# Performance work log

Measured on AMD Instinct MI355X. Metric: run time of the kernel, lower is better.

Reference implementation:

```python
import jax, jax.numpy as jnp
import numpy as np

N, D, H = 4096, 1024, 16
HD = D // H  # 64
EPS = 1e-5


def setup_inputs() -> dict:
    key = jax.random.key(0)
    ks = jax.random.split(key, 12)
    lim = 1.0 / np.sqrt(D)
    def lin(kw, kb):
        W = jax.random.uniform(kw, (D, D), jnp.float32, -lim, lim)
        b = jax.random.uniform(kb, (D,), jnp.float32, -lim, lim)
        return W, b
    Wq, bq = lin(ks[0], ks[1])
    Wk, bk = lin(ks[2], ks[3])
    Wv, bv = lin(ks[4], ks[5])
    Wo, bo = lin(ks[6], ks[7])
    return {
        "query": jax.random.normal(ks[8], (N, D), jnp.float32),
        "key": jax.random.normal(ks[9], (N, D), jnp.float32),
        "value": jax.random.normal(ks[10], (N, D), jnp.float32),
        "Wq": Wq, "bq": bq, "Wk": Wk, "bk": bk,
        "Wv": Wv, "bv": bv, "Wo": Wo, "bo": bo,
        "q_norm_w": jnp.ones((HD,), jnp.float32),
        "k_norm_w": jnp.ones((HD,), jnp.float32),
    }


def _rmsnorm(x, w):
    # eqx.nn.RMSNorm: weight-only, eps=1e-5, over last dim
    inv = jax.lax.rsqrt(jnp.mean(x * x, axis=-1, keepdims=True) + EPS)
    return w * x * inv


def reference(query, key, value, Wq, bq, Wk, bk, Wv, bv, Wo, bo, q_norm_w, k_norm_w):
    n = query.shape[0]
    q = (query @ Wq.T + bq).reshape(n, H, HD)
    k = (key @ Wk.T + bk).reshape(n, H, HD)
    v = (value @ Wv.T + bv).reshape(n, H, HD)
    q = _rmsnorm(q, q_norm_w)
    k = _rmsnorm(k, k_norm_w)
    # scale=1.0: raw unscaled dot-product logits
    logits = jnp.einsum('qhd,khd->hqk', q, k)  # [H, N, N]
    probs = jax.nn.softmax(logits, axis=-1)
    attn = jnp.einsum('hqk,khd->qhd', probs, v).reshape(n, H * HD)
    return attn @ Wo.T + bo
```

## Files before the change

### kernel.cpp

```cpp
#include <hip/hip_runtime.h>
#include <stdint.h>
#include <stddef.h>

#define N_TOK 4096
#define DM    1024
#define NHEAD 16
#define HD    64

typedef __attribute__((ext_vector_type(8)))  short bf16x8;
typedef __attribute__((ext_vector_type(4)))  short bf16x4;
typedef __attribute__((ext_vector_type(4)))  float f32x4;
typedef __attribute__((ext_vector_type(16))) float f32x16;

static __device__ __forceinline__ float bf2f(short u) {
  union { unsigned int i; float f; } c;
  c.i = ((unsigned int)(unsigned short)u) << 16;
  return c.f;
}
static __device__ __forceinline__ unsigned short f2bf(float f) {
  union { float f; unsigned int i; } c; c.f = f;
  unsigned int x = c.i;
  return (unsigned short)((x + 0x7fffu + ((x >> 16) & 1u)) >> 16);
}
static __device__ __forceinline__ unsigned int cvtpk(float lo, float hi) {
  unsigned int d;
  asm("v_cvt_pk_bf16_f32 %0, %1, %2" : "=v"(d) : "v"(lo), "v"(hi));
  return d;
}
static __device__ __forceinline__ void plswap(unsigned int& a, unsigned int& b) {
  asm("v_permlane32_swap_b32 %0, %1" : "+v"(a), "+v"(b));
}
#if __has_builtin(__builtin_amdgcn_exp2f)
#define EXP2(x) __builtin_amdgcn_exp2f(x)
#else
#define EXP2(x) exp2f(x)
#endif
static __device__ __forceinline__ void gload16(const void* g, void* l) {
  __builtin_amdgcn_global_load_lds(
      (const __attribute__((address_space(1))) unsigned int*)g,
      (__attribute__((address_space(3))) unsigned int*)l, 16, 0, 0);
}

struct Cvt7 { const float* s[7]; unsigned short* d[7]; };
__global__ void cvt_all(Cvt7 a) {
  int u0 = blockIdx.x << 10;
  int seg, off;
  if (u0 < 1572864) { seg = u0 >> 19; off = u0 & 524287; }
  else { int j = u0 - 1572864; seg = 3 + (j >> 17); off = j & 131071; }
  const float* s = a.s[seg];
  unsigned short* dd = a.d[seg];
  int t = off + threadIdx.x;
#pragma unroll
  for (int j = 0; j < 4; ++j, t += 256) {
    const f32x4* sp = (const f32x4*)(s + (size_t)t * 8);
    f32x4 x = sp[0], y = sp[1];
    bf16x8 o;
    o[0] = (short)f2bf(x[0]); o[1] = (short)f2bf(x[1]);
    o[2] = (short)f2bf(x[2]); o[3] = (short)f2bf(x[3]);
    o[4] = (short)f2bf(y[0]); o[5] = (short)f2bf(y[1]);
    o[6] = (short)f2bf(y[2]); o[7] = (short)f2bf(y[3]);
    *(bf16x8*)(dd + (size_t)t * 8) = o;
  }
}

template <int MI>
static __device__ __forceinline__ void gemm_core(
    const unsigned short* __restrict__ A,
    const unsigned short* __restrict__ W,
    const float* __restrict__ bias,
    unsigned short* __restrict__ Cb,
    float* __restrict__ Cf,
    const float* __restrict__ nw,
    int Nn, int K, int mode, int m0, int n0)
{
  __shared__ __align__(16) unsigned short At[2][MI * 1024];
  __shared__ __align__(16) unsigned short Wt[2][128 * 32];
  const int tid  = threadIdx.x;
  const int wid  = tid >> 6, lane = tid & 63;
  const int lm   = lane & 15, lg = lane >> 4;
  const int wm   = (wid >> 1) * (MI * 16), wn = (wid & 1) * 64;
  const int CPW  = (MI * 2 + 8) / 4;

  f32x4 acc[MI][4];
#pragma unroll
  for (int i = 0; i < MI; ++i)
#pragma unroll
    for (int j = 0; j < 4; ++j) acc[i][j] = f32x4{0.f, 0.f, 0.f, 0.f};

  auto stage = [&](int b, int k0) {
#pragma unroll
    for (int i = 0; i < CPW; ++i) {
      int c = wid * CPW + i;
      if (c < MI * 2)
        gload16(A + (size_t)(m0 + c * 16 + (lane >> 2)) * K + k0 + (lane & 3) * 8,
                (char*)At + b * (MI * 2048) + c * 1024);
      else
        gload16(W + (size_t)(n0 + (c - MI * 2) * 16 + (lane >> 2)) * K + k0 + (lane & 3) * 8,
                (char*)Wt + b * 8192 + (c - MI * 2) * 1024);
    }
  };

  const int nk = K >> 5;
  stage(0, 0);
  __syncthreads();
  for (int kt = 0; kt < nk; ++kt) {
    const int cur = kt & 1;
    if (kt + 1 < nk) stage(cur ^ 1, (kt + 1) << 5);

    bf16x8 af[MI], bfr[4];
#pragma unroll
    for (int mi = 0; mi < MI; ++mi)
      af[mi] = *(const bf16x8*)&At[cur][(wm + mi * 16 + lm) * 32 + lg * 8];
#pragma unroll
    for (int ni = 0; ni < 4; ++ni)
      bfr[ni] = *(const bf16x8*)&Wt[cur][(wn + ni * 16 + lm) * 32 + lg * 8];
    __builtin_amdgcn_s_setprio(1);
#pragma unroll
    for (int mi = 0; mi < MI; ++mi)
#pragma unroll
      for (int ni = 0; ni < 4; ++ni)
        acc[mi][ni] = __builtin_amdgcn_mfma_f32_16x16x32_bf16(
            af[mi], bfr[ni], acc[mi][ni], 0, 0, 0);
    __builtin_amdgcn_s_setprio(0);
    __syncthreads();
  }

  float bv[4];
#pragma unroll
  for (int ni = 0; ni < 4; ++ni) bv[ni] = bias[n0 + wn + ni * 16 + lm];

  if (mode <= 1) {
#pragma unroll
    for (int mi = 0; mi < MI; ++mi)
#pragma unroll
      for (int ni = 0; ni < 4; ++ni) {
        int n = n0 + wn + ni * 16 + lm;
#pragma unroll
        for (int r = 0; r < 4; ++r) {
          int m = m0 + wm + mi * 16 + lg * 4 + r;
          float v = acc[mi][ni][r] + bv[ni];
          if (mode == 1) Cf[(size_t)m * Nn + n] = v;
          else           Cb[(size_t)m * Nn + n] = f2bf(v);
        }
      }
  } else if (mode == 2) {
    const int h = (n0 + wn) >> 6;
    float w_[4];
#pragma unroll
    for (int ni = 0; ni < 4; ++ni) w_[ni] = nw[ni * 16 + lm];
#pragma unroll
    for (int mi = 0; mi < MI; ++mi) {
      float t[4][4], ssq[4];
#pragma unroll
      for (int ni = 0; ni < 4; ++ni)
#pragma unroll
        for (int r = 0; r < 4; ++r) t[ni][r] = acc[mi][ni][r] + bv[ni];
#pragma unroll
      for (int r = 0; r < 4; ++r)
        ssq[r] = t[0][r]*t[0][r] + t[1][r]*t[1][r] + t[2][r]*t[2][r] + t[3][r]*t[3][r];
#pragma unroll
      for (int r = 0; r < 4; ++r) {
        ssq[r] += __shfl_xor(ssq[r], 1);
        ssq[r] += __shfl_xor(ssq[r], 2);
        ssq[r] += __shfl_xor(ssq[r], 4);
        ssq[r] += __shfl_xor(ssq[r], 8);
      }
#pragma unroll
      for (int r = 0; r < 4; ++r) {
        float iv = rsqrtf(ssq[r] * (1.f / 64.f) + 1e-5f);
        int n_ = m0 + wm + mi * 16 + lg * 4 + r;
#pragma unroll
        for (int ni = 0; ni < 4; ++ni) {
          int d = ni * 16 + lm;
          Cb[(size_t)h * (N_TOK * HD) + (size_t)n_ * HD + d] = f2bf(t[ni][r] * w_[ni] * iv);
        }
      }
    }
  } else {
    const int h = (n0 + wn) >> 6;
#pragma unroll
    for (int mi = 0; mi < MI; ++mi)
#pragma unroll
      for (int ni = 0; ni < 4; ++ni) {
        int d  = ni * 16 + lm;
        int nb = m0 + wm + mi * 16 + lg * 4;
        bf16x4 o;
#pragma unroll
        for (int r = 0; r < 4; ++r) o[r] = (short)f2bf(acc[mi][ni][r] + bv[ni]);
        *(bf16x4*)&Cb[(size_t)h * (HD * N_TOK) + (size_t)d * N_TOK + nb] = o;
      }
  }
}

__global__ __launch_bounds__(256, 3) void qkv_gemm(
    const unsigned short* __restrict__ a0, const unsigned short* __restrict__ a1,
    const unsigned short* __restrict__ a2,
    const unsigned short* __restrict__ w0, const unsigned short* __restrict__ w1,
    const unsigned short* __restrict__ w2,
    const float* __restrict__ b0, const float* __restrict__ b1,
    const float* __restrict__ b2,
    unsigned short* __restrict__ o0, unsigned short* __restrict__ o1,
    unsigned short* __restrict__ o2,
    const float* __restrict__ knw)
{
  const int z = blockIdx.z;
  const unsigned short* A = (z == 0) ? a0 : (z == 1) ? a1 : a2;
  const unsigned short* W = (z == 0) ? w0 : (z == 1) ? w1 : w2;
  const float* B          = (z == 0) ? b0 : (z == 1) ? b1 : b2;
  unsigned short* O       = (z == 0) ? o0 : (z == 1) ? o1 : o2;
  const int mode          = (z == 0) ? 0 : (z == 1) ? 2 : 3;
  gemm_core<4>(A, W, B, O, nullptr, knw, DM, DM, mode,
               blockIdx.y * 128, blockIdx.x * 128);
}

__global__ __launch_bounds__(256, 3) void out_gemm(
    const unsigned short* __restrict__ A, const unsigned short* __restrict__ W,
    const float* __restrict__ bias, float* __restrict__ Cf)
{
  gemm_core<4>(A, W, bias, nullptr, Cf, nullptr, DM, DM, 1,
               blockIdx.y * 128, blockIdx.x * 128);
}

__global__ __launch_bounds__(512, 4) void attn_kernel(
    const unsigned short* __restrict__ qb,
    const unsigned short* __restrict__ kn,
    const unsigned short* __restrict__ vt,
    const float* __restrict__ wq,
    unsigned short* __restrict__ ob)
{
  __shared__ __align__(16) unsigned short SM[2][2][2][4096];

  const int wg   = blockIdx.x;
  const int x_   = wg & 7, rest = wg >> 3;
  const int h    = x_ * 2 + (rest & 1);
  const int qt   = rest >> 1;
  const int tid  = threadIdx.x;
  const int wid  = tid >> 6, lane = tid & 63;
  const int g    = wid >> 2, wv = wid & 3;
  const int l31  = lane & 31, hi = lane >> 5;
  const int sl   = l31 & 7;
  const int qbase = qt * 128 + wv * 32;

  bf16x8 qf[4];
  {
    const unsigned short* qp = qb + (size_t)(qbase + l31) * DM + h * HD + hi * 8;
    float qv[32]; float ss = 0.f;
#pragma unroll
    for (int s = 0; s < 4; ++s) {
      bf16x8 raw = *(const bf16x8*)(qp + s * 16);
#pragma unroll
      for (int j = 0; j < 8; ++j) { float f = bf2f(raw[j]); qv[s*8+j] = f; ss += f*f; }
    }
    ss += __shfl_xor(ss, 32);
    float inv = rsqrtf(ss * (1.f / 64.f) + 1e-5f) * 1.44269504f;
#pragma unroll
    for (int s = 0; s < 4; ++s)
#pragma unroll
      for (int j = 0; j < 8; ++j)
        qf[s][j] = (short)f2bf(qv[s*8+j] * wq[s*16 + hi*8 + j] * inv);
  }

  int slot[4];
#pragma unroll
  for (int x = 0; x < 4; ++x) slot[x] = (((2*x + hi) ^ sl) << 4);
  const char* base = (const char*)SM + g * 32768 + l31 * 128;

  const char* gsrc[4];
  char*       ldst[4];
  long        gstep[4];
  {
    const char* knb = (const char*)kn + (size_t)h * (N_TOK * HD * 2);
    const char* vtb = (const char*)vt + (size_t)h * (HD * N_TOK * 2);
    char* smG = (char*)SM + g * 32768;
#pragma unroll
    for (int i = 0; i < 4; ++i) {
      int chunk = wv * 4 + i;
      int off   = (chunk & 7) * 1024 + lane * 16;
      int row   = off >> 7;
      int scol  = (off & 127) ^ ((row & 7) << 4);
      if (chunk < 8) {
        gsrc[i]  = knb + (size_t)(g * 2048 + row) * 128 + scol;
        gstep[i] = 64 * 128;
        ldst[i]  = smG + (chunk & 7) * 1024;
      } else {
        gsrc[i]  = vtb + (size_t)row * (N_TOK * 2) + g * 4096 + scol;
        gstep[i] = 64 * 2;
        ldst[i]  = smG + 8192 + (chunk & 7) * 1024;
      }
    }
  }

  f32x16 oacc[2], fz;
#pragma unroll
  for (int r = 0; r < 16; ++r) { oacc[0][r] = 0.f; oacc[1][r] = 0.f; fz[r] = 0.f; }
  float lsp[4] = {0.f, 0.f, 0.f, 0.f};

#pragma unroll
  for (int i = 0; i < 4; ++i) { gload16(gsrc[i], ldst[i]); gsrc[i] += gstep[i]; }
  __syncthreads();

  const int NT = 2048 / 64;
  for (int it = 0; it < NT; ++it) {
    const int cur = it & 1;
    if (it + 1 < NT) {
      const int nb = cur ^ 1;
#pragma unroll
      for (int i = 0; i < 4; ++i) {
        gload16(gsrc[i], ldst[i] + nb * 16384);
        gsrc[i] += gstep[i];
      }
    }
    const char* KB = base + cur * 16384;
    const char* VB = KB + 8192;

#pragma unroll
    for (int kt = 0; kt < 2; ++kt) {
      __builtin_amdgcn_s_setprio(1);
      bf16x8 kf0 = *(const bf16x8*)(KB + kt * 4096 + slot[0]);
      f32x16 sc = __builtin_amdgcn_mfma_f32_32x32x16_bf16(kf0, qf[0], fz, 0, 0, 0);
#pragma unroll
      for (int s = 1; s < 4; ++s) {
        bf16x8 kf = *(const bf16x8*)(KB + kt * 4096 + slot[s]);
        sc = __builtin_amdgcn_mfma_f32_32x32x16_bf16(kf, qf[s], sc, 0, 0, 0);
      }
      __builtin_amdgcn_s_setprio(0);
      float e[16];
#pragma unroll
      for (int r = 0; r < 16; ++r) { e[r] = EXP2(sc[r]); lsp[r & 3] += e[r]; }
      unsigned int wpk[4][2];
#pragma unroll
      for (int b = 0; b < 4; ++b) {
        wpk[b][0] = cvtpk(e[4*b+0], e[4*b+1]);
        wpk[b][1] = cvtpk(e[4*b+2], e[4*b+3]);
      }
#pragma unroll
      for (int pr = 0; pr < 2; ++pr) {
        unsigned int x0 = wpk[2*pr][0], x1 = wpk[2*pr][1];
        unsigned int y0 = wpk[2*pr+1][0], y1 = wpk[2*pr+1][1];
        plswap(x0, y0);
        plswap(x1, y1);
        union { unsigned int u[4]; bf16x8 v; } pa;
        pa.u[0] = x0; pa.u[1] = x1; pa.u[2] = y0; pa.u[3] = y1;
        int ks = kt * 2 + pr;
        __builtin_amdgcn_s_setprio(1);
#pragma unroll
        for (int dt = 0; dt < 2; ++dt) {
          bf16x8 vf = *(const bf16x8*)(VB + dt * 4096 + slot[ks]);
          oacc[dt] = __builtin_amdgcn_mfma_f32_32x32x16_bf16(pa.v, vf, oacc[dt], 0, 0, 0);
        }
        __builtin_amdgcn_s_setprio(0);
      }
    }
    __syncthreads();
  }

  float ls = (lsp[0] + lsp[1]) + (lsp[2] + lsp[3]);
  ls += __shfl_xor(ls, 32);

  float* ex  = (float*)((char*)SM + 32768);
  float* lsx = (float*)SM;
  const int idx = wv * 64 + lane;
  if (g == 1) {
#pragma unroll
    for (int dt = 0; dt < 2; ++dt)
#pragma unroll
      for (int r = 0; r < 16; ++r)
        ex[(dt * 16 + r) * 256 + idx] = oacc[dt][r];
    lsx[idx] = ls;
  }
  __syncthreads();
  if (g == 0) {
#pragma unroll
    for (int dt = 0; dt < 2; ++dt)
#pragma unroll
      for (int r = 0; r < 16; ++r)
        oacc[dt][r] += ex[(dt * 16 + r) * 256 + idx];
    ls += lsx[idx];
    float il = 1.f / ls;
#pragma unroll
    for (int r = 0; r < 16; ++r) {
      int q = (r & 3) + 8 * (r >> 2) + 4 * hi;
      float ilr = __int_as_float(
          __builtin_amdgcn_ds_bpermute(q << 2, __float_as_int(il)));
      unsigned short* op = ob + (size_t)(qbase + q) * DM + h * HD + l31;
      op[0]  = f2bf(oacc[0][r] * ilr);
      op[32] = f2bf(oacc[1][r] * ilr);
    }
  }
}

extern "C" void kernel_launch(void* const* d_in, const int* in_sizes, int n_in,
                              void* d_out, int out_size, void* d_ws, size_t ws_size,
                              hipStream_t stream) {
  const float* query = (const float*)d_in[0];
  const float* key   = (const float*)d_in[1];
  const float* value = (const float*)d_in[2];
  const float* Wq    = (const float*)d_in[3];
  const float* bq    = (const float*)d_in[4];
  const float* Wk    = (const float*)d_in[5];
  const float* bk    = (const float*)d_in[6];
  const float* Wv    = (const float*)d_in[7];
  const float* bv    = (const float*)d_in[8];
  const float* Wo    = (const float*)d_in[9];
  const float* bo    = (const float*)d_in[10];
  const float* qnw   = (const float*)d_in[11];
  const float* knw   = (const float*)d_in[12];

  char* ws = (char*)d_ws;
  const size_t MB = 1024 * 1024;
  unsigned short* qpj = (unsigned short*)(ws + 0 * MB);
  unsigned short* Kn  = (unsigned short*)(ws + 8 * MB);
  unsigned short* Vt  = (unsigned short*)(ws + 16 * MB);
  unsigned short* wob = (unsigned short*)(ws + 24 * MB);
  unsigned short* wqb = (unsigned short*)(ws + 26 * MB);
  unsigned short* wkb = (unsigned short*)(ws + 28 * MB);
  unsigned short* wvb = (unsigned short*)(ws + 30 * MB);
  unsigned short* qbf = (unsigned short*)(ws + 32 * MB);
  unsigned short* kbf = (unsigned short*)(ws + 40 * MB);
  unsigned short* vbf = (unsigned short*)(ws + 48 * MB);
  unsigned short* apj = (unsigned short*)(ws + 56 * MB);

  Cvt7 ca;
  ca.s[0] = query; ca.d[0] = qbf;
  ca.s[1] = key;   ca.d[1] = kbf;
  ca.s[2] = value; ca.d[2] = vbf;
  ca.s[3] = Wq;    ca.d[3] = wqb;
  ca.s[4] = Wk;    ca.d[4] = wkb;
  ca.s[5] = Wv;    ca.d[5] = wvb;
  ca.s[6] = Wo;    ca.d[6] = wob;
  cvt_all<<<2048, 256, 0, stream>>>(ca);

  qkv_gemm<<<dim3(DM / 128, N_TOK / 128, 3), 256, 0, stream>>>(
      qbf, kbf, vbf, wqb, wkb, wvb, bq, bk, bv, qpj, Kn, Vt, knw);

  attn_kernel<<<512, 512, 0, stream>>>(qpj, Kn, Vt, qnw, apj);

  out_gemm<<<dim3(DM / 128, N_TOK / 128), 256, 0, stream>>>(apj, wob, bo, (float*)d_out);
}
```

Measured before the change: 152.2 us.

## Split attention KV range across separate blocks and merge partials in new kernel

Attention workgroups no longer hold two 4-wave groups that split the KV range and reduce through shared memory. Each 256-thread block now handles one KV half, so twice as many smaller blocks launch, and unnormalized bf16 partial outputs and row sums go to workspace. A new merge kernel adds the two partials and normalizes them. The aim is higher occupancy and no in-block reduction barrier, at the cost of an extra launch, extra global traffic for the partials, and rounding the partials to bf16 before the sum.

```diff
diff --git a/kernel.cpp b/kernel.cpp
--- a/kernel.cpp
+++ b/kernel.cpp
@@ -221,25 +221,26 @@
                blockIdx.y * 128, blockIdx.x * 128);
 }
 
-__global__ __launch_bounds__(512, 4) void attn_kernel(
+__global__ __launch_bounds__(256, 5) void attn_kernel(
     const unsigned short* __restrict__ qb,
     const unsigned short* __restrict__ kn,
     const unsigned short* __restrict__ vt,
     const float* __restrict__ wq,
-    unsigned short* __restrict__ ob)
+    unsigned short* __restrict__ opart,
+    float* __restrict__ lpart)
 {
-  __shared__ __align__(16) unsigned short SM[2][2][2][4096];
+  __shared__ __align__(16) unsigned short SM[2][2][4096];
 
   const int wg   = blockIdx.x;
   const int x_   = wg & 7, rest = wg >> 3;
   const int h    = x_ * 2 + (rest & 1);
-  const int qt   = rest >> 1;
+  const int sp   = (rest >> 1) & 1;
+  const int qt   = rest >> 2;
   const int tid  = threadIdx.x;
   const int wid  = tid >> 6, lane = tid & 63;
-  const int g    = wid >> 2, wv = wid & 3;
   const int l31  = lane & 31, hi = lane >> 5;
   const int sl   = l31 & 7;
-  const int qbase = qt * 128 + wv * 32;
+  const int qbase = qt * 128 + wid * 32;
 
   bf16x8 qf[4];
   {
@@ -263,7 +264,7 @@
   int slot[4];
 #pragma unroll
   for (int x = 0; x < 4; ++x) slot[x] = (((2*x + hi) ^ sl) << 4);
-  const char* base = (const char*)SM + g * 32768 + l31 * 128;
+  const char* base = (const char*)SM + l31 * 128;
 
   const char* gsrc[4];
   char*       ldst[4];
@@ -271,21 +272,20 @@
   {
     const char* knb = (const char*)kn + (size_t)h * (N_TOK * HD * 2);
     const char* vtb = (const char*)vt + (size_t)h * (HD * N_TOK * 2);
-    char* smG = (char*)SM + g * 32768;
 #pragma unroll
     for (int i = 0; i < 4; ++i) {
-      int chunk = wv * 4 + i;
+      int chunk = wid * 4 + i;
       int off   = (chunk & 7) * 1024 + lane * 16;
       int row   = off >> 7;
       int scol  = (off & 127) ^ ((row & 7) << 4);
       if (chunk < 8) {
-        gsrc[i]  = knb + (size_t)(g * 2048 + row) * 128 + scol;
+        gsrc[i]  = knb + (size_t)(sp * 2048 + row) * 128 + scol;
         gstep[i] = 64 * 128;
-        ldst[i]  = smG + (chunk & 7) * 1024;
+        ldst[i]  = (char*)SM + (chunk & 7) * 1024;
       } else {
-        gsrc[i]  = vtb + (size_t)row * (N_TOK * 2) + g * 4096 + scol;
+        gsrc[i]  = vtb + (size_t)row * (N_TOK * 2) + sp * 4096 + scol;
         gstep[i] = 64 * 2;
-        ldst[i]  = smG + 8192 + (chunk & 7) * 1024;
+        ldst[i]  = (char*)SM + 8192 + (chunk & 7) * 1024;
       }
     }
   }
@@ -356,37 +356,33 @@
 
   float ls = (lsp[0] + lsp[1]) + (lsp[2] + lsp[3]);
   ls += __shfl_xor(ls, 32);
-
-  float* ex  = (float*)((char*)SM + 32768);
-  float* lsx = (float*)SM;
-  const int idx = wv * 64 + lane;
-  if (g == 1) {
-#pragma unroll
-    for (int dt = 0; dt < 2; ++dt)
-#pragma unroll
-      for (int r = 0; r < 16; ++r)
-        ex[(dt * 16 + r) * 256 + idx] = oacc[dt][r];
-    lsx[idx] = ls;
-  }
-  __syncthreads();
-  if (g == 0) {
-#pragma unroll
-    for (int dt = 0; dt < 2; ++dt)
-#pragma unroll
-      for (int r = 0; r < 16; ++r)
-        oacc[dt][r] += ex[(dt * 16 + r) * 256 + idx];
-    ls += lsx[idx];
-    float il = 1.f / ls;
-#pragma unroll
-    for (int r = 0; r < 16; ++r) {
-      int q = (r & 3) + 8 * (r >> 2) + 4 * hi;
-      float ilr = __int_as_float(
-          __builtin_amdgcn_ds_bpermute(q << 2, __float_as_int(il)));
-      unsigned short* op = ob + (size_t)(qbase + q) * DM + h * HD + l31;
-      op[0]  = f2bf(oacc[0][r] * ilr);
-      op[32] = f2bf(oacc[1][r] * ilr);
-    }
-  }
+  unsigned short* Opb = opart + (size_t)sp * (N_TOK * DM);
+#pragma unroll
+  for (int r = 0; r < 16; ++r) {
+    int q = (r & 3) + 8 * (r >> 2) + 4 * hi;
+    unsigned short* p = Opb + (size_t)(qbase + q) * DM + h * HD + l31;
+    p[0]  = f2bf(oacc[0][r]);
+    p[32] = f2bf(oacc[1][r]);
+  }
+  if (hi == 0)
+    lpart[(size_t)sp * (NHEAD * N_TOK) + h * N_TOK + qbase + l31] = ls;
+}
+
+__global__ void merge_kernel(const unsigned short* __restrict__ opart,
+                             const float* __restrict__ lpart,
+                             unsigned short* __restrict__ am)
+{
+  int i = (blockIdx.x * 256 + threadIdx.x) * 8;
+  int n = i >> 10, c = i & 1023, h = c >> 6;
+  float l = lpart[h * N_TOK + n] + lpart[NHEAD * N_TOK + h * N_TOK + n];
+  float il = 1.f / l;
+  bf16x8 a = *(const bf16x8*)(opart + (size_t)n * DM + c);
+  bf16x8 b = *(const bf16x8*)(opart + (size_t)(N_TOK * DM) + (size_t)n * DM + c);
+  bf16x8 o;
+#pragma unroll
+  for (int j = 0; j < 8; ++j)
+    o[j] = (short)f2bf((bf2f(a[j]) + bf2f(b[j])) * il);
+  *(bf16x8*)(am + i) = o;
 }
 
 extern "C" void kernel_launch(void* const* d_in, const int* in_sizes, int n_in,
@@ -419,6 +415,8 @@
   unsigned short* kbf = (unsigned short*)(ws + 40 * MB);
   unsigned short* vbf = (unsigned short*)(ws + 48 * MB);
   unsigned short* apj = (unsigned short*)(ws + 56 * MB);
+  unsigned short* Op  = (unsigned short*)(ws + 32 * MB);
+  float*          Lp  = (float*)(ws + 48 * MB);
 
   Cvt7 ca;
   ca.s[0] = query; ca.d[0] = qbf;
@@ -433,7 +431,9 @@
   qkv_gemm<<<dim3(DM / 128, N_TOK / 128, 3), 256, 0, stream>>>(
       qbf, kbf, vbf, wqb, wkb, wvb, bq, bk, bv, qpj, Kn, Vt, knw);
 
-  attn_kernel<<<512, 512, 0, stream>>>(qpj, Kn, Vt, qnw, apj);
+  attn_kernel<<<1024, 256, 0, stream>>>(qpj, Kn, Vt, qnw, Op, Lp);
+
+  merge_kernel<<<N_TOK * DM / 8 / 256, 256, 0, stream>>>(Op, Lp, apj);
 
   out_gemm<<<dim3(DM / 128, N_TOK / 128), 256, 0, stream>>>(apj, wob, bo, (float*)d_out);
 }
```

After: 168.3 us. 10.6% more time.

## Fuse fp32-to-bf16 activation conversion into QKV GEMM tile loads

Applied to the files above, without the earlier changes.

The QKV projection GEMM now loads fp32 query/key/value tiles straight into LDS using an XOR-swizzled layout and converts them to bf16 in registers with v_cvt_pk_bf16_f32 before the MFMA. The standalone conversion kernel now only handles the four weight matrices. This drops one full read and write pass over the 48 MB of activations. In exchange the A tile in LDS is twice as large, which may lower occupancy, and the GEMM loads twice the A bytes from global memory, since each tile is re-read for every N block.

```diff
diff --git a/kernel.cpp b/kernel.cpp
--- a/kernel.cpp
+++ b/kernel.cpp
@@ -41,12 +41,10 @@
       (__attribute__((address_space(3))) unsigned int*)l, 16, 0, 0);
 }
 
-struct Cvt7 { const float* s[7]; unsigned short* d[7]; };
-__global__ void cvt_all(Cvt7 a) {
+struct Cvt4 { const float* s[4]; unsigned short* d[4]; };
+__global__ void cvt_w(Cvt4 a) {
   int u0 = blockIdx.x << 10;
-  int seg, off;
-  if (u0 < 1572864) { seg = u0 >> 19; off = u0 & 524287; }
-  else { int j = u0 - 1572864; seg = 3 + (j >> 17); off = j & 131071; }
+  int seg = u0 >> 17, off = u0 & 131071;
   const float* s = a.s[seg];
   unsigned short* dd = a.d[seg];
   int t = off + threadIdx.x;
@@ -63,9 +61,10 @@
   }
 }
 
-template <int MI>
+template <int MI, bool AF32>
 static __device__ __forceinline__ void gemm_core(
     const unsigned short* __restrict__ A,
+    const float* __restrict__ A32,
     const unsigned short* __restrict__ W,
     const float* __restrict__ bias,
     unsigned short* __restrict__ Cb,
@@ -73,13 +72,15 @@
     const float* __restrict__ nw,
     int Nn, int K, int mode, int m0, int n0)
 {
-  __shared__ __align__(16) unsigned short At[2][MI * 1024];
+  __shared__ __align__(16) unsigned short At[2][MI * (AF32 ? 2048 : 1024)];
   __shared__ __align__(16) unsigned short Wt[2][128 * 32];
   const int tid  = threadIdx.x;
   const int wid  = tid >> 6, lane = tid & 63;
   const int lm   = lane & 15, lg = lane >> 4;
   const int wm   = (wid >> 1) * (MI * 16), wn = (wid & 1) * 64;
-  const int CPW  = (MI * 2 + 8) / 4;
+  const int NCA  = AF32 ? MI * 4 : MI * 2;
+  const int CPW  = (NCA + 8) / 4;
+  const int ABUF = MI * (AF32 ? 4096 : 2048);
 
   f32x4 acc[MI][4];
 #pragma unroll
@@ -91,12 +92,22 @@
 #pragma unroll
     for (int i = 0; i < CPW; ++i) {
       int c = wid * CPW + i;
-      if (c < MI * 2)
-        gload16(A + (size_t)(m0 + c * 16 + (lane >> 2)) * K + k0 + (lane & 3) * 8,
-                (char*)At + b * (MI * 2048) + c * 1024);
-      else
-        gload16(W + (size_t)(n0 + (c - MI * 2) * 16 + (lane >> 2)) * K + k0 + (lane & 3) * 8,
-                (char*)Wt + b * 8192 + (c - MI * 2) * 1024);
+      if (c < NCA) {
+        if constexpr (AF32) {
+          int off  = c * 1024 + lane * 16;
+          int row  = off >> 7;
+          int scol = (off & 127) ^ ((row & 7) << 4);
+          gload16(A32 + (size_t)(m0 + row) * K + k0 + (scol >> 2),
+                  (char*)At + b * ABUF + c * 1024);
+        } else {
+          gload16(A + (size_t)(m0 + c * 16 + (lane >> 2)) * K + k0 + (lane & 3) * 8,
+                  (char*)At + b * ABUF + c * 1024);
+        }
+      } else {
+        int cw = c - NCA;
+        gload16(W + (size_t)(n0 + cw * 16 + (lane >> 2)) * K + k0 + (lane & 3) * 8,
+                (char*)Wt + b * 8192 + cw * 1024);
+      }
     }
   };
 
@@ -109,8 +120,21 @@
 
     bf16x8 af[MI], bfr[4];
 #pragma unroll
-    for (int mi = 0; mi < MI; ++mi)
-      af[mi] = *(const bf16x8*)&At[cur][(wm + mi * 16 + lm) * 32 + lg * 8];
+    for (int mi = 0; mi < MI; ++mi) {
+      if constexpr (AF32) {
+        int arow = wm + mi * 16 + lm;
+        const char* ab = (char*)At + cur * ABUF + arow * 128;
+        int swz = (arow & 7) << 4;
+        f32x4 a0 = *(const f32x4*)(ab + ((lg * 32) ^ swz));
+        f32x4 a1 = *(const f32x4*)(ab + ((lg * 32 + 16) ^ swz));
+        union { unsigned int u[4]; bf16x8 v; } p;
+        p.u[0] = cvtpk(a0[0], a0[1]); p.u[1] = cvtpk(a0[2], a0[3]);
+        p.u[2] = cvtpk(a1[0], a1[1]); p.u[3] = cvtpk(a1[2], a1[3]);
+        af[mi] = p.v;
+      } else {
+        af[mi] = *(const bf16x8*)&At[cur][(wm + mi * 16 + lm) * 32 + lg * 8];
+      }
+    }
 #pragma unroll
     for (int ni = 0; ni < 4; ++ni)
       bfr[ni] = *(const bf16x8*)&Wt[cur][(wn + ni * 16 + lm) * 32 + lg * 8];
@@ -193,8 +217,8 @@
 }
 
 __global__ __launch_bounds__(256, 3) void qkv_gemm(
-    const unsigned short* __restrict__ a0, const unsigned short* __restrict__ a1,
-    const unsigned short* __restrict__ a2,
+    const float* __restrict__ a0, const float* __restrict__ a1,
+    const float* __restrict__ a2,
     const unsigned short* __restrict__ w0, const unsigned short* __restrict__ w1,
     const unsigned short* __restrict__ w2,
     const float* __restrict__ b0, const float* __restrict__ b1,
@@ -204,21 +228,21 @@
     const float* __restrict__ knw)
 {
   const int z = blockIdx.z;
-  const unsigned short* A = (z == 0) ? a0 : (z == 1) ? a1 : a2;
+  const float* A32        = (z == 0) ? a0 : (z == 1) ? a1 : a2;
   const unsigned short* W = (z == 0) ? w0 : (z == 1) ? w1 : w2;
   const float* B          = (z == 0) ? b0 : (z == 1) ? b1 : b2;
   unsigned short* O       = (z == 0) ? o0 : (z == 1) ? o1 : o2;
   const int mode          = (z == 0) ? 0 : (z == 1) ? 2 : 3;
-  gemm_core<4>(A, W, B, O, nullptr, knw, DM, DM, mode,
-               blockIdx.y * 128, blockIdx.x * 128);
+  gemm_core<4, true>(nullptr, A32, W, B, O, nullptr, knw, DM, DM, mode,
+                     blockIdx.y * 128, blockIdx.x * 128);
 }
 
 __global__ __launch_bounds__(256, 3) void out_gemm(
     const unsigned short* __restrict__ A, const unsigned short* __restrict__ W,
     const float* __restrict__ bias, float* __restrict__ Cf)
 {
-  gemm_core<4>(A, W, bias, nullptr, Cf, nullptr, DM, DM, 1,
-               blockIdx.y * 128, blockIdx.x * 128);
+  gemm_core<4, false>(A, nullptr, W, bias, nullptr, Cf, nullptr, DM, DM, 1,
+                      blockIdx.y * 128, blockIdx.x * 128);
 }
 
 __global__ __launch_bounds__(512, 4) void attn_kernel(
@@ -415,23 +439,17 @@
   unsigned short* wqb = (unsigned short*)(ws + 26 * MB);
   unsigned short* wkb = (unsigned short*)(ws + 28 * MB);
   unsigned short* wvb = (unsigned short*)(ws + 30 * MB);
-  unsigned short* qbf = (unsigned short*)(ws + 32 * MB);
-  unsigned short* kbf = (unsigned short*)(ws + 40 * MB);
-  unsigned short* vbf = (unsigned short*)(ws + 48 * MB);
   unsigned short* apj = (unsigned short*)(ws + 56 * MB);
 
-  Cvt7 ca;
-  ca.s[0] = query; ca.d[0] = qbf;
-  ca.s[1] = key;   ca.d[1] = kbf;
-  ca.s[2] = value; ca.d[2] = vbf;
-  ca.s[3] = Wq;    ca.d[3] = wqb;
-  ca.s[4] = Wk;    ca.d[4] = wkb;
-  ca.s[5] = Wv;    ca.d[5] = wvb;
-  ca.s[6] = Wo;    ca.d[6] = wob;
-  cvt_all<<<2048, 256, 0, stream>>>(ca);
+  Cvt4 ca;
+  ca.s[0] = Wq; ca.d[0] = wqb;
+  ca.s[1] = Wk; ca.d[1] = wkb;
+  ca.s[2] = Wv; ca.d[2] = wvb;
+  ca.s[3] = Wo; ca.d[3] = wob;
+  cvt_w<<<512, 256, 0, stream>>>(ca);
 
   qkv_gemm<<<dim3(DM / 128, N_TOK / 128, 3), 256, 0, stream>>>(
-      qbf, kbf, vbf, wqb, wkb, wvb, bq, bk, bv, qpj, Kn, Vt, knw);
+      query, key, value, wqb, wkb, wvb, bq, bk, bv, qpj, Kn, Vt, knw);
 
   attn_kernel<<<512, 512, 0, stream>>>(qpj, Kn, Vt, qnw, apj);
 
```

New measurement: 165.5 us. 1.09x slower.
